# Kernel optimization log

Measured on AMD Instinct MI355X. Metric: run time of the kernel, lower is better.

The kernel has to match this reference:

```python
import jax, jax.numpy as jnp
import numpy as np

NF, NX, GROUP_SIZE = 8192, 2048, 64
N_GROUPS = NX // GROUP_SIZE  # pad = 0 since NX % GROUP_SIZE == 0


def setup_inputs() -> dict:
    key = jax.random.key(0)
    k1, k2, k3, k4, k5 = jax.random.split(key, 5)
    x = jax.random.normal(k1, (4, 2048, NX), dtype=jnp.float32)
    packed = jax.random.randint(k2, (NF, NX // 2), 0, 256, dtype=jnp.int32)
    scales = jax.random.uniform(k3, (NF, N_GROUPS), dtype=jnp.float32)
    zeros = jax.random.randint(k4, (NF, N_GROUPS), 0, 16, dtype=jnp.int32)
    bias = jax.random.normal(k5, (NF,), dtype=jnp.float32)
    return {"x": x, "packed": packed, "scales": scales, "zeros": zeros, "bias": bias}


def _dequantize(packed, scales, zeros):
    # packed: [nf, nx//2] bytes, two int4 nibbles per byte (low nibble first)
    low = packed & 15
    high = (packed >> 4) & 15
    # interleave: q[:, 0::2] = low, q[:, 1::2] = high
    q = jnp.stack([low, high], axis=-1).reshape(NF, NX).astype(jnp.float32)
    q = q.reshape(NF, N_GROUPS, GROUP_SIZE)
    W = (q - zeros.astype(jnp.float32)[:, :, None]) * scales[:, :, None]
    return W.reshape(NF, NX)  # [nf, nx]


def reference(x, packed, scales, zeros, bias):
    W = _dequantize(packed, scales, zeros).astype(x.dtype)  # [nf, nx]
    size_out = x.shape[:-1] + (NF,)
    out = jnp.matmul(x.reshape(-1, NX), W.T) + bias  # addmm
    return out.reshape(size_out)
```

## Files before the change

kernel.cpp:

```cpp
#include <hip/hip_runtime.h>
#include <stdint.h>

#define NF 8192
#define NX 2048
#define MROWS 8192
#define NGROUPS 32
#define NT 32

typedef unsigned short u16;
typedef __bf16 bf16x8 __attribute__((ext_vector_type(8)));
typedef float f32x4 __attribute__((ext_vector_type(4)));

#define AS1 __attribute__((address_space(1)))
#define AS3 __attribute__((address_space(3)))

__device__ __forceinline__ void glds16(const void* g, void* l) {
    __builtin_amdgcn_global_load_lds((AS1 void*)(uintptr_t)g,
                                     (AS3 void*)(uintptr_t)l, 16, 0, 0);
}

__device__ __forceinline__ u16 f2bf(float f) {
    unsigned u = __float_as_uint(f);
    return (u16)((u + 0x7FFFu + ((u >> 16) & 1u)) >> 16);
}

__global__ void dequant_kernel(const int* __restrict__ packed,
                               const float* __restrict__ scales,
                               const int* __restrict__ zeros,
                               uint32_t* __restrict__ W2) {
    int tid = blockIdx.x * blockDim.x + threadIdx.x;
    int f = tid >> 10;
    int i = tid & 1023;
    int g = f * NGROUPS + (i >> 5);
    int p = packed[tid];
    float s = scales[g];
    float z = (float)zeros[g];
    float w0 = ((float)(p & 15) - z) * s;
    float w1 = ((float)((p >> 4) & 15) - z) * s;
    W2[tid] = (uint32_t)f2bf(w0) | ((uint32_t)f2bf(w1) << 16);
}

__global__ void cvt_kernel(const float4* __restrict__ x, ushort4* __restrict__ y) {
    int i = blockIdx.x * blockDim.x + threadIdx.x;
    float4 v = x[i];
    ushort4 o;
    o.x = f2bf(v.x); o.y = f2bf(v.y); o.z = f2bf(v.z); o.w = f2bf(v.w);
    y[i] = o;
}


#define BAR    __builtin_amdgcn_s_barrier()
#define LGKM8  asm volatile("s_waitcnt lgkmcnt(8)" ::: "memory")
#define LGKM0  asm volatile("s_waitcnt lgkmcnt(0)" ::: "memory")
#define VMCNT0 asm volatile("s_waitcnt vmcnt(0)" ::: "memory")
#define FENCE  __builtin_amdgcn_sched_barrier(0)

#define LD8(off) (*(const bf16x8*)(smem + (off)))

#define MFMA(d, va, vb) d = __builtin_amdgcn_mfma_f32_16x16x32_bf16(va, vb, d, 0, 0, 0)

#define STAGE8(BUF, KOFF) do { \
    glds16(srcA + (KOFF),          smem + (BUF) + t16); \
    glds16(srcA + 262144 + (KOFF), smem + (BUF) + 8192  + t16); \
    glds16(srcA + 524288 + (KOFF), smem + (BUF) + 16384 + t16); \
    glds16(srcA + 786432 + (KOFF), smem + (BUF) + 24576 + t16); \
    glds16(srcB + (KOFF),          smem + (BUF) + 32768 + t16); \
    glds16(srcB + 262144 + (KOFF), smem + (BUF) + 40960 + t16); \
    glds16(srcB + 524288 + (KOFF), smem + (BUF) + 49152 + t16); \
    glds16(srcB + 786432 + (KOFF), smem + (BUF) + 57344 + t16); \
} while (0)

__global__ __launch_bounds__(512, 2)
void gemm_kernel(const u16* __restrict__ A, const u16* __restrict__ B,
                 const float* __restrict__ bias, float* __restrict__ C) {
    __shared__ __align__(16) char smem[131072];

    const int t = threadIdx.x;

    const int bid = blockIdx.x;
    const int xcd = bid & 7;
    const int local = bid >> 3;
    const int super = local >> 6;
    const int r = local & 63;
    const int by = xcd * 4 + super * 2 + (r & 1);
    const int bx = r >> 1;
    const int rowA0 = by * 256;
    const int rowB0 = bx * 256;

    const int t16 = t * 16;
    const int ulog = (t & 7) ^ ((t >> 3) & 7);
    const int koffS = (ulog >> 2) * 64 + (ulog & 3) * 16;
    const char* srcA = (const char*)A + (size_t)(rowA0 + (t >> 3)) * 4096 + koffS;
    const char* srcB = (const char*)B + (size_t)(rowB0 + (t >> 3)) * 4096 + koffS;

    const int lane = t & 63;
    const int wv = t >> 6;
    const int wm = wv >> 2;
    const int wn = wv & 3;
    const int l15 = lane & 15;
    const int quad = lane >> 4;
    const int l7 = l15 & 7;
    const int sx0 = (quad ^ l7) << 4;
    const int sx1 = ((4 + quad) ^ l7) << 4;
    const int aOff = (wm * 128 + l15) * 128;
    const int bOff = 32768 + (wn * 64 + l15) * 128;

    f32x4 acc[8][4];
#pragma unroll
    for (int i = 0; i < 8; ++i)
#pragma unroll
        for (int j = 0; j < 4; ++j) acc[i][j] = {0.f, 0.f, 0.f, 0.f};

    bf16x8 a0[8], a1[8], b0[4], b1[4];

    STAGE8(0, 0);
    VMCNT0;

#pragma unroll 1
    for (int T = 0; T < NT; ++T) {
        const int bo = (T & 1) << 16;
        const int so = bo ^ 65536;

        FENCE; BAR; FENCE;
#pragma unroll
        for (int i = 0; i < 8; ++i) a0[i] = LD8(bo + aOff + i * 2048 + sx0);
#pragma unroll
        for (int j = 0; j < 4; ++j) b0[j] = LD8(bo + bOff + j * 2048 + sx0);
        FENCE;
        if (T + 1 < NT) STAGE8(so, (T + 1) * 128);
        FENCE;
#pragma unroll
        for (int i = 0; i < 8; ++i) a1[i] = LD8(bo + aOff + i * 2048 + sx1);
        FENCE; LGKM8; FENCE;
        __builtin_amdgcn_s_setprio(1);
#pragma unroll
        for (int j = 0; j < 2; ++j)
#pragma unroll
            for (int i = 0; i < 8; ++i) MFMA(acc[i][j], a0[i], b0[j]);
        __builtin_amdgcn_s_setprio(0);
        FENCE;
#pragma unroll
        for (int j = 0; j < 4; ++j) b1[j] = LD8(bo + bOff + j * 2048 + sx1);
        FENCE;
        __builtin_amdgcn_s_setprio(1);
#pragma unroll
        for (int j = 2; j < 4; ++j)
#pragma unroll
            for (int i = 0; i < 8; ++i) MFMA(acc[i][j], a0[i], b0[j]);
        __builtin_amdgcn_s_setprio(0);
        FENCE; LGKM0; FENCE;
        __builtin_amdgcn_s_setprio(1);
#pragma unroll
        for (int j = 0; j < 4; ++j)
#pragma unroll
            for (int i = 0; i < 8; ++i) MFMA(acc[i][j], a1[i], b1[j]);
        __builtin_amdgcn_s_setprio(0);
        FENCE;
        if (T + 1 < NT) VMCNT0;
    }

    const int col0 = rowB0 + wn * 64 + l15;
    const int row0 = rowA0 + wm * 128 + quad * 4;
    float bj[4];
#pragma unroll
    for (int j = 0; j < 4; ++j) bj[j] = bias[col0 + j * 16];
#pragma unroll
    for (int i = 0; i < 8; ++i) {
#pragma unroll
        for (int e = 0; e < 4; ++e) {
            float* crow = C + (size_t)(row0 + i * 16 + e) * NF;
#pragma unroll
            for (int j = 0; j < 4; ++j)
                __builtin_nontemporal_store(acc[i][j][e] + bj[j], crow + col0 + j * 16);
        }
    }
}

extern "C" void kernel_launch(void* const* d_in, const int* in_sizes, int n_in,
                              void* d_out, int out_size, void* d_ws, size_t ws_size,
                              hipStream_t stream) {
    const float* x      = (const float*)d_in[0];
    const int* packed   = (const int*)d_in[1];
    const float* scales = (const float*)d_in[2];
    const int* zeros    = (const int*)d_in[3];
    const float* bias   = (const float*)d_in[4];
    float* out = (float*)d_out;

    u16* Wq = (u16*)d_ws;
    u16* Xb = Wq + (size_t)NF * NX;

    dequant_kernel<<<(NF * (NX / 2)) / 256, 256, 0, stream>>>(packed, scales, zeros, (uint32_t*)Wq);
    cvt_kernel<<<(MROWS * NX / 4) / 256, 256, 0, stream>>>((const float4*)x, (ushort4*)Xb);

    gemm_kernel<<<dim3((MROWS / 256) * (NF / 256)), 512, 0, stream>>>(Xb, Wq, bias, out);
}
```

Baseline: 284.5 us.

## Fuse fp32-to-bf16 activation conversion into GEMM A-tile staging

Removes the separate cvt kernel. The GEMM now loads fp32 activations directly into registers, converts them to bf16 and writes them to LDS in the swizzled layout, interleaved with the MFMA phases. This drops a full pass over x (read fp32, write bf16) and one launch. In exchange, the GEMM reads twice as many bytes for A, each 256-row tile re-reads and re-converts fp32 data across all 32 column tiles, and the pipeline gains register-path stores and extra waitcnts.

```diff
diff --git a/kernel.cpp b/kernel.cpp
--- a/kernel.cpp
+++ b/kernel.cpp
@@ -40,18 +40,12 @@
     W2[tid] = (uint32_t)f2bf(w0) | ((uint32_t)f2bf(w1) << 16);
 }
 
-__global__ void cvt_kernel(const float4* __restrict__ x, ushort4* __restrict__ y) {
-    int i = blockIdx.x * blockDim.x + threadIdx.x;
-    float4 v = x[i];
-    ushort4 o;
-    o.x = f2bf(v.x); o.y = f2bf(v.y); o.z = f2bf(v.z); o.w = f2bf(v.w);
-    y[i] = o;
-}
-
 
 #define BAR    __builtin_amdgcn_s_barrier()
 #define LGKM8  asm volatile("s_waitcnt lgkmcnt(8)" ::: "memory")
+#define LGKM2  asm volatile("s_waitcnt lgkmcnt(2)" ::: "memory")
 #define LGKM0  asm volatile("s_waitcnt lgkmcnt(0)" ::: "memory")
+#define VMC4   asm volatile("s_waitcnt vmcnt(4)" ::: "memory")
 #define VMCNT0 asm volatile("s_waitcnt vmcnt(0)" ::: "memory")
 #define FENCE  __builtin_amdgcn_sched_barrier(0)
 
@@ -59,19 +53,24 @@
 
 #define MFMA(d, va, vb) d = __builtin_amdgcn_mfma_f32_16x16x32_bf16(va, vb, d, 0, 0, 0)
 
-#define STAGE8(BUF, KOFF) do { \
-    glds16(srcA + (KOFF),          smem + (BUF) + t16); \
-    glds16(srcA + 262144 + (KOFF), smem + (BUF) + 8192  + t16); \
-    glds16(srcA + 524288 + (KOFF), smem + (BUF) + 16384 + t16); \
-    glds16(srcA + 786432 + (KOFF), smem + (BUF) + 24576 + t16); \
+#define STAGEB(BUF, KOFF) do { \
     glds16(srcB + (KOFF),          smem + (BUF) + 32768 + t16); \
     glds16(srcB + 262144 + (KOFF), smem + (BUF) + 40960 + t16); \
     glds16(srcB + 524288 + (KOFF), smem + (BUF) + 49152 + t16); \
     glds16(srcB + 786432 + (KOFF), smem + (BUF) + 57344 + t16); \
 } while (0)
 
+#define CW(c_, v0_, v1_) do { \
+    bf16x8 w_; \
+    w_[0] = (__bf16)v0_.x; w_[1] = (__bf16)v0_.y; \
+    w_[2] = (__bf16)v0_.z; w_[3] = (__bf16)v0_.w; \
+    w_[4] = (__bf16)v1_.x; w_[5] = (__bf16)v1_.y; \
+    w_[6] = (__bf16)v1_.z; w_[7] = (__bf16)v1_.w; \
+    *(bf16x8*)(dstA + (c_) * 8192) = w_; \
+} while (0)
+
 __global__ __launch_bounds__(512, 2)
-void gemm_kernel(const u16* __restrict__ A, const u16* __restrict__ B,
+void gemm_kernel(const float* __restrict__ X, const u16* __restrict__ B,
                  const float* __restrict__ bias, float* __restrict__ C) {
     __shared__ __align__(16) char smem[131072];
 
@@ -90,8 +89,12 @@
     const int t16 = t * 16;
     const int ulog = (t & 7) ^ ((t >> 3) & 7);
     const int koffS = (ulog >> 2) * 64 + (ulog & 3) * 16;
-    const char* srcA = (const char*)A + (size_t)(rowA0 + (t >> 3)) * 4096 + koffS;
     const char* srcB = (const char*)B + (size_t)(rowB0 + (t >> 3)) * 4096 + koffS;
+
+    const int u = t & 7;
+    const char* srcX = (const char*)X + (size_t)(rowA0 + (t >> 3)) * 8192
+                       + (u >> 2) * 128 + (u & 3) * 32;
+    const int aW = (t >> 3) * 128 + ulog * 16;
 
     const int lane = t & 63;
     const int wv = t >> 6;
@@ -112,22 +115,50 @@
         for (int j = 0; j < 4; ++j) acc[i][j] = {0.f, 0.f, 0.f, 0.f};
 
     bf16x8 a0[8], a1[8], b0[4], b1[4];
-
-    STAGE8(0, 0);
-    VMCNT0;
+    float4 xv0, xv1, xv2, xv3;
+
+    {
+        char* dstA = smem + aW;
+        xv0 = *(const float4*)(srcX);
+        xv1 = *(const float4*)(srcX + 16);
+        xv2 = *(const float4*)(srcX + 524288);
+        xv3 = *(const float4*)(srcX + 524288 + 16);
+        FENCE;
+        STAGEB(0, 0);
+        FENCE; VMC4; FENCE;
+        CW(0, xv0, xv1); CW(1, xv2, xv3);
+        xv0 = *(const float4*)(srcX + 1048576);
+        xv1 = *(const float4*)(srcX + 1048576 + 16);
+        xv2 = *(const float4*)(srcX + 1572864);
+        xv3 = *(const float4*)(srcX + 1572864 + 16);
+        FENCE; VMCNT0; FENCE;
+        CW(2, xv0, xv1); CW(3, xv2, xv3);
+        LGKM0;
+    }
+
+    int kN = 256;
 
 #pragma unroll 1
     for (int T = 0; T < NT; ++T) {
         const int bo = (T & 1) << 16;
         const int so = bo ^ 65536;
+        const bool more = (T + 1 < NT);
+        char* dstA = smem + so + aW;
 
         FENCE; BAR; FENCE;
+        if (more) {
+            xv0 = *(const float4*)(srcX + kN);
+            xv1 = *(const float4*)(srcX + kN + 16);
+            xv2 = *(const float4*)(srcX + 524288 + kN);
+            xv3 = *(const float4*)(srcX + 524288 + kN + 16);
+            FENCE;
+            STAGEB(so, kN >> 1);
+            FENCE;
+        }
 #pragma unroll
         for (int i = 0; i < 8; ++i) a0[i] = LD8(bo + aOff + i * 2048 + sx0);
 #pragma unroll
         for (int j = 0; j < 4; ++j) b0[j] = LD8(bo + bOff + j * 2048 + sx0);
-        FENCE;
-        if (T + 1 < NT) STAGE8(so, (T + 1) * 128);
         FENCE;
 #pragma unroll
         for (int i = 0; i < 8; ++i) a1[i] = LD8(bo + aOff + i * 2048 + sx1);
@@ -148,7 +179,18 @@
 #pragma unroll
             for (int i = 0; i < 8; ++i) MFMA(acc[i][j], a0[i], b0[j]);
         __builtin_amdgcn_s_setprio(0);
-        FENCE; LGKM0; FENCE;
+        FENCE;
+        if (more) {
+            VMC4; FENCE;
+            CW(0, xv0, xv1); CW(1, xv2, xv3);
+            xv0 = *(const float4*)(srcX + 1048576 + kN);
+            xv1 = *(const float4*)(srcX + 1048576 + kN + 16);
+            xv2 = *(const float4*)(srcX + 1572864 + kN);
+            xv3 = *(const float4*)(srcX + 1572864 + kN + 16);
+            FENCE; LGKM2; FENCE;
+        } else {
+            LGKM0; FENCE;
+        }
         __builtin_amdgcn_s_setprio(1);
 #pragma unroll
         for (int j = 0; j < 4; ++j)
@@ -156,7 +198,12 @@
             for (int i = 0; i < 8; ++i) MFMA(acc[i][j], a1[i], b1[j]);
         __builtin_amdgcn_s_setprio(0);
         FENCE;
-        if (T + 1 < NT) VMCNT0;
+        if (more) {
+            VMCNT0; FENCE;
+            CW(2, xv0, xv1); CW(3, xv2, xv3);
+            LGKM0; FENCE;
+            kN += 256;
+        }
     }
 
     const int col0 = rowB0 + wn * 64 + l15;
@@ -187,10 +234,8 @@
     float* out = (float*)d_out;
 
     u16* Wq = (u16*)d_ws;
-    u16* Xb = Wq + (size_t)NF * NX;
 
     dequant_kernel<<<(NF * (NX / 2)) / 256, 256, 0, stream>>>(packed, scales, zeros, (uint32_t*)Wq);
-    cvt_kernel<<<(MROWS * NX / 4) / 256, 256, 0, stream>>>((const float4*)x, (ushort4*)Xb);
-
-    gemm_kernel<<<dim3((MROWS / 256) * (NF / 256)), 512, 0, stream>>>(Xb, Wq, bias, out);
-}
+
+    gemm_kernel<<<dim3((MROWS / 256) * (NF / 256)), 512, 0, stream>>>(x, Wq, bias, out);
+}
```

Measured after the change: 327.3 us. 1.15x slower.
